# Kernel optimization log

Measured on AMD Instinct MI355X. Metric: run time of the kernel, lower is better.

## Reference

```python
import jax, jax.numpy as jnp
import numpy as np
import math

INPUT_DIM = 1024
OUTPUT_DIM = 8192
M_BLOCKS = 8  # ceil(OUTPUT_DIM / INPUT_DIM)
SCALE = 1.0


def fwht(x):
    """Unnormalized fast Walsh-Hadamard transform over the last axis.
    Matches the torch recursive-cat implementation (Sylvester/natural order).
    """
    n = x.shape[-1]
    lead = x.shape[:-1]
    h = 1
    while h < n:
        y = x.reshape(lead + (n // (2 * h), 2, h))
        a = y[..., 0, :]
        b = y[..., 1, :]
        x = jnp.stack([a + b, a - b], axis=-2).reshape(lead + (n,))
        h *= 2
    return x


def setup_inputs() -> dict:
    key = jax.random.key(0)
    kx, kb, kg, ks, kp, ku = jax.random.split(key, 6)
    x = jax.random.normal(kx, (8, 1024, INPUT_DIM), dtype=jnp.float32)
    B = jax.random.normal(kb, (M_BLOCKS, INPUT_DIM), dtype=jnp.float32)
    G = jax.random.normal(kg, (M_BLOCKS, INPUT_DIM), dtype=jnp.float32)
    S = jax.random.uniform(ks, (M_BLOCKS, INPUT_DIM), dtype=jnp.float32)
    P = jax.random.randint(kp, (M_BLOCKS, INPUT_DIM), 0, INPUT_DIM, dtype=jnp.int64)
    u_rand = jax.random.uniform(ku, (OUTPUT_DIM,), dtype=jnp.float32)
    return {"x": x, "B": B, "G": G, "S": S, "P": P, "u_rand": u_rand}


def reference(x, B, G, S, P, u_rand):
    d = INPUT_DIM
    # flatten all leading dims into rows: (R, 1, d)
    xr = x.reshape(-1, 1, d)
    Bx = xr * B                                   # (R, m, d)
    HBx = fwht(Bx)                                # (R, m, d)
    idx = jnp.broadcast_to(P[None], HBx.shape)    # per-block permutation gather
    PHBx = jnp.take_along_axis(HBx, idx, axis=-1)
    GPHBx = PHBx * G
    HGPHBx = fwht(GPHBx)
    SHGPHBx = HGPHBx * S
    norm_factor = 1.0 / (SCALE * math.sqrt(d))
    Vx = norm_factor * SHGPHBx.reshape(SHGPHBx.shape[0], -1)  # (R, m*d)
    result = Vx[:, :OUTPUT_DIM]
    # phi nonlinearity: cos(x + 2*pi*U) * sqrt(2/output_dim)
    phase = (2.0 * jnp.pi) * u_rand
    result = jnp.cos(result + phase) * math.sqrt(2.0 / OUTPUT_DIM)
    return result
```

## Files before the change

kernel.cpp:

```cpp
#include <hip/hip_runtime.h>
#include <math.h>


typedef unsigned uint2_ev __attribute__((ext_vector_type(2)));
typedef float    f32x4    __attribute__((ext_vector_type(4)));

template <int CTRL>
__device__ __forceinline__ float dpp_f(float x) {
    return __int_as_float(
        __builtin_amdgcn_mov_dpp(__float_as_int(x), CTRL, 0xF, 0xF, true));
}

#define DPP_XOR1 0xB1
#define DPP_XOR2 0x4E
#define DPP_XOR3 0x1B
#define DPP_HMIR 0x141
#define DPP_ROR8 0x128

__device__ __forceinline__ void fwht_full(float v[16], float sg0, float sg1,
                                          float sg2, float sg3, float sg4,
                                          float sg5) {
    (void)sg4; (void)sg5;
#pragma unroll
    for (int h = 1; h < 16; h <<= 1) {
#pragma unroll
        for (int k = 0; k < 16; ++k) {
            if (!(k & h)) {
                float a = v[k], b = v[k ^ h];
                v[k] = a + b;
                v[k ^ h] = a - b;
            }
        }
    }
#pragma unroll
    for (int k = 0; k < 16; ++k) v[k] = fmaf(v[k], sg0, dpp_f<DPP_XOR1>(v[k]));
#pragma unroll
    for (int k = 0; k < 16; ++k) v[k] = fmaf(v[k], sg1, dpp_f<DPP_XOR2>(v[k]));
#pragma unroll
    for (int k = 0; k < 16; ++k)
        v[k] = fmaf(v[k], sg2, dpp_f<DPP_XOR3>(dpp_f<DPP_HMIR>(v[k])));
#pragma unroll
    for (int k = 0; k < 16; ++k) v[k] = fmaf(v[k], sg3, dpp_f<DPP_ROR8>(v[k]));

#if __has_builtin(__builtin_amdgcn_permlane16_swap)
#pragma unroll
    for (int p = 0; p < 8; ++p) {
        uint2_ev r = __builtin_amdgcn_permlane16_swap(
            __float_as_uint(v[2 * p]), __float_as_uint(v[2 * p + 1]), false,
            false);
        float s = __uint_as_float(r.x) + __uint_as_float(r.y);
        float d = __uint_as_float(r.x) - __uint_as_float(r.y);
        uint2_ev q = __builtin_amdgcn_permlane16_swap(
            __float_as_uint(s), __float_as_uint(d), false, false);
        v[2 * p]     = __uint_as_float(q.x);
        v[2 * p + 1] = __uint_as_float(q.y);
    }
#else
#pragma unroll
    for (int k = 0; k < 16; ++k) {
        float t = __int_as_float(
            __builtin_amdgcn_ds_swizzle(__float_as_int(v[k]), 0x401F));
        v[k] = fmaf(v[k], sg4, t);
    }
#endif

#if __has_builtin(__builtin_amdgcn_permlane32_swap)
#pragma unroll
    for (int p = 0; p < 8; ++p) {
        uint2_ev r = __builtin_amdgcn_permlane32_swap(
            __float_as_uint(v[2 * p]), __float_as_uint(v[2 * p + 1]), false,
            false);
        float s = __uint_as_float(r.x) + __uint_as_float(r.y);
        float d = __uint_as_float(r.x) - __uint_as_float(r.y);
        uint2_ev q = __builtin_amdgcn_permlane32_swap(
            __float_as_uint(s), __float_as_uint(d), false, false);
        v[2 * p]     = __uint_as_float(q.x);
        v[2 * p + 1] = __uint_as_float(q.y);
    }
#else
#pragma unroll
    for (int k = 0; k < 16; ++k) {
        float t = __shfl_xor(v[k], 32, 64);
        v[k] = fmaf(v[k], sg5, t);
    }
#endif
}

__global__ __launch_bounds__(256) void fastfood_kernel(
    const float* __restrict__ x, const float* __restrict__ B,
    const float* __restrict__ G, const float* __restrict__ S,
    const int* __restrict__ P, const float* __restrict__ u_rand,
    float* __restrict__ out)
{
    __shared__ float lds[4 * 1088];
    const int lane = threadIdx.x & 63;
    const int wv   = threadIdx.x >> 6;
    const int row  = blockIdx.x * 4 + wv;

    const float sg0 = (lane & 1)  ? -1.f : 1.f;
    const float sg1 = (lane & 2)  ? -1.f : 1.f;
    const float sg2 = (lane & 4)  ? -1.f : 1.f;
    const float sg3 = (lane & 8)  ? -1.f : 1.f;
    const float sg4 = (lane & 16) ? -1.f : 1.f;
    const float sg5 = (lane & 32) ? -1.f : 1.f;

    float* wlds = lds + wv * 1088;
    float4* w4L1 = (float4*)(wlds + 16 * lane + 4 * (lane >> 2));

    const float c_arg = 0.03125f * 0.15915494309189535f;
    const float c_amp = 0.015625f;

    float xv[16];
    {
        const f32x4* x4 =
            (const f32x4*)(x + (size_t)row * 1024 + 16 * lane);
#pragma unroll
        for (int j = 0; j < 4; ++j) {
            f32x4 t = __builtin_nontemporal_load(&x4[j]);
            xv[4 * j + 0] = t.x; xv[4 * j + 1] = t.y;
            xv[4 * j + 2] = t.z; xv[4 * j + 3] = t.w;
        }
    }

#pragma unroll 1
    for (int m = 0; m < 8; ++m) {
        const int mo = m * 1024;
        float v[16];

        {
            const float4* B4 = (const float4*)(B + mo + 16 * lane);
#pragma unroll
            for (int j = 0; j < 4; ++j) {
                float4 b = B4[j];
                v[4 * j + 0] = xv[4 * j + 0] * b.x;
                v[4 * j + 1] = xv[4 * j + 1] * b.y;
                v[4 * j + 2] = xv[4 * j + 2] * b.z;
                v[4 * j + 3] = xv[4 * j + 3] * b.w;
            }
        }

        fwht_full(v, sg0, sg1, sg2, sg3, sg4, sg5);

        const int4*   P4 = (const int4*)(P + mo);
        const float4* G4 = (const float4*)(G + mo);
        int4   pj[4];
        float4 gj[4];
#pragma unroll
        for (int j = 0; j < 4; ++j) {
            pj[j] = P4[64 * j + lane];
            gj[j] = G4[64 * j + lane];
        }

#pragma unroll
        for (int j = 0; j < 4; ++j)
            w4L1[j] = make_float4(v[4 * j + 0], v[4 * j + 1],
                                  v[4 * j + 2], v[4 * j + 3]);

#pragma unroll
        for (int j = 0; j < 4; ++j) {
            int4 p = pj[j];
            float4 g = gj[j];
            v[4 * j + 0] = wlds[p.x + ((p.x >> 6) << 2)] * g.x;
            v[4 * j + 1] = wlds[p.y + ((p.y >> 6) << 2)] * g.y;
            v[4 * j + 2] = wlds[p.z + ((p.z >> 6) << 2)] * g.z;
            v[4 * j + 3] = wlds[p.w + ((p.w >> 6) << 2)] * g.w;
        }

        fwht_full(v, sg0, sg1, sg2, sg3, sg4, sg5);

        {
            const float4* S4 = (const float4*)(S + mo);
            const float4* U4 = (const float4*)(u_rand + mo);
            f32x4* o4 = (f32x4*)(out + (size_t)row * 8192 + mo);
#pragma unroll
            for (int b = 0; b < 4; ++b) {
                int idx = b * 64 + lane;
                float4 sv = S4[idx], uv = U4[idx];
                f32x4 rr;
                rr.x = __builtin_amdgcn_cosf(__builtin_amdgcn_fractf(
                           fmaf(v[4 * b + 0] * sv.x, c_arg, uv.x))) * c_amp;
                rr.y = __builtin_amdgcn_cosf(__builtin_amdgcn_fractf(
                           fmaf(v[4 * b + 1] * sv.y, c_arg, uv.y))) * c_amp;
                rr.z = __builtin_amdgcn_cosf(__builtin_amdgcn_fractf(
                           fmaf(v[4 * b + 2] * sv.z, c_arg, uv.z))) * c_amp;
                rr.w = __builtin_amdgcn_cosf(__builtin_amdgcn_fractf(
                           fmaf(v[4 * b + 3] * sv.w, c_arg, uv.w))) * c_amp;
                __builtin_nontemporal_store(rr, &o4[idx]);
            }
        }
    }
}

extern "C" void kernel_launch(void* const* d_in, const int* in_sizes, int n_in,
                              void* d_out, int out_size, void* d_ws, size_t ws_size,
                              hipStream_t stream) {
    const float* x = (const float*)d_in[0];
    const float* B = (const float*)d_in[1];
    const float* G = (const float*)d_in[2];
    const float* S = (const float*)d_in[3];
    const int*   P = (const int*)d_in[4];
    const float* u = (const float*)d_in[5];
    float* out = (float*)d_out;

    dim3 grid(2048), block(256);
    hipLaunchKernelGGL(fastfood_kernel, grid, block, 0, stream,
                       x, B, G, S, P, u, out);
}
```

Baseline: 345.3 us.

## Process two rows per wavefront to share B/P/G/S/U loads and add ILP

Each wavefront now handles two rows at once, interleaving their Walsh-Hadamard transforms so the per-block B, P, G, S and u_rand loads are shared and the DPP/permlane chains of the two rows can overlap. The grid is halved, LDS per block doubles, and launch bounds now request 3 blocks per CU. The aim is fewer redundant parameter loads and more instruction-level parallelism to hide shuffle latency. In exchange, register pressure rises and occupancy may drop. The non-permlane fallback paths are also removed.

```diff
diff --git a/kernel.cpp b/kernel.cpp
--- a/kernel.cpp
+++ b/kernel.cpp
@@ -17,129 +17,138 @@
 #define DPP_HMIR 0x141
 #define DPP_ROR8 0x128
 
-__device__ __forceinline__ void fwht_full(float v[16], float sg0, float sg1,
-                                          float sg2, float sg3, float sg4,
-                                          float sg5) {
-    (void)sg4; (void)sg5;
+__device__ __forceinline__ void pl16_pair(float& e0, float& e1) {
+    uint2_ev r = __builtin_amdgcn_permlane16_swap(
+        __float_as_uint(e0), __float_as_uint(e1), false, false);
+    float s = __uint_as_float(r.x) + __uint_as_float(r.y);
+    float d = __uint_as_float(r.x) - __uint_as_float(r.y);
+    uint2_ev q = __builtin_amdgcn_permlane16_swap(
+        __float_as_uint(s), __float_as_uint(d), false, false);
+    e0 = __uint_as_float(q.x);
+    e1 = __uint_as_float(q.y);
+}
+
+__device__ __forceinline__ void pl32_pair(float& e0, float& e1) {
+    uint2_ev r = __builtin_amdgcn_permlane32_swap(
+        __float_as_uint(e0), __float_as_uint(e1), false, false);
+    float s = __uint_as_float(r.x) + __uint_as_float(r.y);
+    float d = __uint_as_float(r.x) - __uint_as_float(r.y);
+    uint2_ev q = __builtin_amdgcn_permlane32_swap(
+        __float_as_uint(s), __float_as_uint(d), false, false);
+    e0 = __uint_as_float(q.x);
+    e1 = __uint_as_float(q.y);
+}
+
+__device__ __forceinline__ void fwht2(float a[16], float b[16], float sg0,
+                                      float sg1, float sg2, float sg3) {
 #pragma unroll
     for (int h = 1; h < 16; h <<= 1) {
 #pragma unroll
         for (int k = 0; k < 16; ++k) {
             if (!(k & h)) {
-                float a = v[k], b = v[k ^ h];
-                v[k] = a + b;
-                v[k ^ h] = a - b;
+                float t0 = a[k], t1 = a[k ^ h];
+                a[k] = t0 + t1;
+                a[k ^ h] = t0 - t1;
+                float u0 = b[k], u1 = b[k ^ h];
+                b[k] = u0 + u1;
+                b[k ^ h] = u0 - u1;
             }
         }
     }
 #pragma unroll
-    for (int k = 0; k < 16; ++k) v[k] = fmaf(v[k], sg0, dpp_f<DPP_XOR1>(v[k]));
-#pragma unroll
-    for (int k = 0; k < 16; ++k) v[k] = fmaf(v[k], sg1, dpp_f<DPP_XOR2>(v[k]));
-#pragma unroll
-    for (int k = 0; k < 16; ++k)
-        v[k] = fmaf(v[k], sg2, dpp_f<DPP_XOR3>(dpp_f<DPP_HMIR>(v[k])));
-#pragma unroll
-    for (int k = 0; k < 16; ++k) v[k] = fmaf(v[k], sg3, dpp_f<DPP_ROR8>(v[k]));
-
-#if __has_builtin(__builtin_amdgcn_permlane16_swap)
+    for (int k = 0; k < 16; ++k) {
+        a[k] = fmaf(a[k], sg0, dpp_f<DPP_XOR1>(a[k]));
+        b[k] = fmaf(b[k], sg0, dpp_f<DPP_XOR1>(b[k]));
+    }
+#pragma unroll
+    for (int k = 0; k < 16; ++k) {
+        a[k] = fmaf(a[k], sg1, dpp_f<DPP_XOR2>(a[k]));
+        b[k] = fmaf(b[k], sg1, dpp_f<DPP_XOR2>(b[k]));
+    }
+#pragma unroll
+    for (int k = 0; k < 16; ++k) {
+        a[k] = fmaf(a[k], sg2, dpp_f<DPP_XOR3>(dpp_f<DPP_HMIR>(a[k])));
+        b[k] = fmaf(b[k], sg2, dpp_f<DPP_XOR3>(dpp_f<DPP_HMIR>(b[k])));
+    }
+#pragma unroll
+    for (int k = 0; k < 16; ++k) {
+        a[k] = fmaf(a[k], sg3, dpp_f<DPP_ROR8>(a[k]));
+        b[k] = fmaf(b[k], sg3, dpp_f<DPP_ROR8>(b[k]));
+    }
 #pragma unroll
     for (int p = 0; p < 8; ++p) {
-        uint2_ev r = __builtin_amdgcn_permlane16_swap(
-            __float_as_uint(v[2 * p]), __float_as_uint(v[2 * p + 1]), false,
-            false);
-        float s = __uint_as_float(r.x) + __uint_as_float(r.y);
-        float d = __uint_as_float(r.x) - __uint_as_float(r.y);
-        uint2_ev q = __builtin_amdgcn_permlane16_swap(
-            __float_as_uint(s), __float_as_uint(d), false, false);
-        v[2 * p]     = __uint_as_float(q.x);
-        v[2 * p + 1] = __uint_as_float(q.y);
-    }
-#else
-#pragma unroll
-    for (int k = 0; k < 16; ++k) {
-        float t = __int_as_float(
-            __builtin_amdgcn_ds_swizzle(__float_as_int(v[k]), 0x401F));
-        v[k] = fmaf(v[k], sg4, t);
-    }
-#endif
-
-#if __has_builtin(__builtin_amdgcn_permlane32_swap)
+        pl16_pair(a[2 * p], a[2 * p + 1]);
+        pl16_pair(b[2 * p], b[2 * p + 1]);
+    }
 #pragma unroll
     for (int p = 0; p < 8; ++p) {
-        uint2_ev r = __builtin_amdgcn_permlane32_swap(
-            __float_as_uint(v[2 * p]), __float_as_uint(v[2 * p + 1]), false,
-            false);
-        float s = __uint_as_float(r.x) + __uint_as_float(r.y);
-        float d = __uint_as_float(r.x) - __uint_as_float(r.y);
-        uint2_ev q = __builtin_amdgcn_permlane32_swap(
-            __float_as_uint(s), __float_as_uint(d), false, false);
-        v[2 * p]     = __uint_as_float(q.x);
-        v[2 * p + 1] = __uint_as_float(q.y);
-    }
-#else
-#pragma unroll
-    for (int k = 0; k < 16; ++k) {
-        float t = __shfl_xor(v[k], 32, 64);
-        v[k] = fmaf(v[k], sg5, t);
-    }
-#endif
-}
-
-__global__ __launch_bounds__(256) void fastfood_kernel(
+        pl32_pair(a[2 * p], a[2 * p + 1]);
+        pl32_pair(b[2 * p], b[2 * p + 1]);
+    }
+}
+
+__global__ __launch_bounds__(256, 3) void fastfood_kernel(
     const float* __restrict__ x, const float* __restrict__ B,
     const float* __restrict__ G, const float* __restrict__ S,
     const int* __restrict__ P, const float* __restrict__ u_rand,
     float* __restrict__ out)
 {
-    __shared__ float lds[4 * 1088];
+    __shared__ float lds[4 * 2176];
     const int lane = threadIdx.x & 63;
     const int wv   = threadIdx.x >> 6;
-    const int row  = blockIdx.x * 4 + wv;
-
-    const float sg0 = (lane & 1)  ? -1.f : 1.f;
-    const float sg1 = (lane & 2)  ? -1.f : 1.f;
-    const float sg2 = (lane & 4)  ? -1.f : 1.f;
-    const float sg3 = (lane & 8)  ? -1.f : 1.f;
-    const float sg4 = (lane & 16) ? -1.f : 1.f;
-    const float sg5 = (lane & 32) ? -1.f : 1.f;
-
-    float* wlds = lds + wv * 1088;
-    float4* w4L1 = (float4*)(wlds + 16 * lane + 4 * (lane >> 2));
+    const int row  = blockIdx.x * 8 + wv * 2;
+
+    const float sg0 = (lane & 1) ? -1.f : 1.f;
+    const float sg1 = (lane & 2) ? -1.f : 1.f;
+    const float sg2 = (lane & 4) ? -1.f : 1.f;
+    const float sg3 = (lane & 8) ? -1.f : 1.f;
+
+    float* ldsA = lds + wv * 2176;
+    float* ldsB = ldsA + 1088;
+    const int woff = 16 * lane + 4 * (lane >> 2);
+    float4* wA = (float4*)(ldsA + woff);
+    float4* wB = (float4*)(ldsB + woff);
 
     const float c_arg = 0.03125f * 0.15915494309189535f;
     const float c_amp = 0.015625f;
 
-    float xv[16];
+    float xvA[16], xvB[16];
     {
-        const f32x4* x4 =
-            (const f32x4*)(x + (size_t)row * 1024 + 16 * lane);
-#pragma unroll
-        for (int j = 0; j < 4; ++j) {
-            f32x4 t = __builtin_nontemporal_load(&x4[j]);
-            xv[4 * j + 0] = t.x; xv[4 * j + 1] = t.y;
-            xv[4 * j + 2] = t.z; xv[4 * j + 3] = t.w;
+        const f32x4* xa = (const f32x4*)(x + (size_t)row * 1024 + 16 * lane);
+        const f32x4* xb = (const f32x4*)(x + (size_t)(row + 1) * 1024 + 16 * lane);
+#pragma unroll
+        for (int j = 0; j < 4; ++j) {
+            f32x4 t = __builtin_nontemporal_load(&xa[j]);
+            xvA[4 * j + 0] = t.x; xvA[4 * j + 1] = t.y;
+            xvA[4 * j + 2] = t.z; xvA[4 * j + 3] = t.w;
+            f32x4 u = __builtin_nontemporal_load(&xb[j]);
+            xvB[4 * j + 0] = u.x; xvB[4 * j + 1] = u.y;
+            xvB[4 * j + 2] = u.z; xvB[4 * j + 3] = u.w;
         }
     }
 
 #pragma unroll 1
     for (int m = 0; m < 8; ++m) {
         const int mo = m * 1024;
-        float v[16];
+        float vA[16], vB[16];
 
         {
             const float4* B4 = (const float4*)(B + mo + 16 * lane);
 #pragma unroll
             for (int j = 0; j < 4; ++j) {
-                float4 b = B4[j];
-                v[4 * j + 0] = xv[4 * j + 0] * b.x;
-                v[4 * j + 1] = xv[4 * j + 1] * b.y;
-                v[4 * j + 2] = xv[4 * j + 2] * b.z;
-                v[4 * j + 3] = xv[4 * j + 3] * b.w;
+                float4 bb = B4[j];
+                vA[4 * j + 0] = xvA[4 * j + 0] * bb.x;
+                vA[4 * j + 1] = xvA[4 * j + 1] * bb.y;
+                vA[4 * j + 2] = xvA[4 * j + 2] * bb.z;
+                vA[4 * j + 3] = xvA[4 * j + 3] * bb.w;
+                vB[4 * j + 0] = xvB[4 * j + 0] * bb.x;
+                vB[4 * j + 1] = xvB[4 * j + 1] * bb.y;
+                vB[4 * j + 2] = xvB[4 * j + 2] * bb.z;
+                vB[4 * j + 3] = xvB[4 * j + 3] * bb.w;
             }
         }
 
-        fwht_full(v, sg0, sg1, sg2, sg3, sg4, sg5);
+        fwht2(vA, vB, sg0, sg1, sg2, sg3);
 
         const int4*   P4 = (const int4*)(P + mo);
         const float4* G4 = (const float4*)(G + mo);
@@ -152,40 +161,61 @@
         }
 
 #pragma unroll
-        for (int j = 0; j < 4; ++j)
-            w4L1[j] = make_float4(v[4 * j + 0], v[4 * j + 1],
-                                  v[4 * j + 2], v[4 * j + 3]);
+        for (int j = 0; j < 4; ++j) {
+            wA[j] = make_float4(vA[4 * j + 0], vA[4 * j + 1],
+                                vA[4 * j + 2], vA[4 * j + 3]);
+            wB[j] = make_float4(vB[4 * j + 0], vB[4 * j + 1],
+                                vB[4 * j + 2], vB[4 * j + 3]);
+        }
 
 #pragma unroll
         for (int j = 0; j < 4; ++j) {
             int4 p = pj[j];
             float4 g = gj[j];
-            v[4 * j + 0] = wlds[p.x + ((p.x >> 6) << 2)] * g.x;
-            v[4 * j + 1] = wlds[p.y + ((p.y >> 6) << 2)] * g.y;
-            v[4 * j + 2] = wlds[p.z + ((p.z >> 6) << 2)] * g.z;
-            v[4 * j + 3] = wlds[p.w + ((p.w >> 6) << 2)] * g.w;
-        }
-
-        fwht_full(v, sg0, sg1, sg2, sg3, sg4, sg5);
+            int o0 = p.x + ((p.x >> 6) << 2);
+            int o1 = p.y + ((p.y >> 6) << 2);
+            int o2 = p.z + ((p.z >> 6) << 2);
+            int o3 = p.w + ((p.w >> 6) << 2);
+            vA[4 * j + 0] = ldsA[o0] * g.x;
+            vA[4 * j + 1] = ldsA[o1] * g.y;
+            vA[4 * j + 2] = ldsA[o2] * g.z;
+            vA[4 * j + 3] = ldsA[o3] * g.w;
+            vB[4 * j + 0] = ldsB[o0] * g.x;
+            vB[4 * j + 1] = ldsB[o1] * g.y;
+            vB[4 * j + 2] = ldsB[o2] * g.z;
+            vB[4 * j + 3] = ldsB[o3] * g.w;
+        }
+
+        fwht2(vA, vB, sg0, sg1, sg2, sg3);
 
         {
             const float4* S4 = (const float4*)(S + mo);
             const float4* U4 = (const float4*)(u_rand + mo);
-            f32x4* o4 = (f32x4*)(out + (size_t)row * 8192 + mo);
+            f32x4* oA = (f32x4*)(out + (size_t)row * 8192 + mo);
+            f32x4* oB = (f32x4*)(out + (size_t)(row + 1) * 8192 + mo);
 #pragma unroll
             for (int b = 0; b < 4; ++b) {
                 int idx = b * 64 + lane;
                 float4 sv = S4[idx], uv = U4[idx];
-                f32x4 rr;
-                rr.x = __builtin_amdgcn_cosf(__builtin_amdgcn_fractf(
-                           fmaf(v[4 * b + 0] * sv.x, c_arg, uv.x))) * c_amp;
-                rr.y = __builtin_amdgcn_cosf(__builtin_amdgcn_fractf(
-                           fmaf(v[4 * b + 1] * sv.y, c_arg, uv.y))) * c_amp;
-                rr.z = __builtin_amdgcn_cosf(__builtin_amdgcn_fractf(
-                           fmaf(v[4 * b + 2] * sv.z, c_arg, uv.z))) * c_amp;
-                rr.w = __builtin_amdgcn_cosf(__builtin_amdgcn_fractf(
-                           fmaf(v[4 * b + 3] * sv.w, c_arg, uv.w))) * c_amp;
-                __builtin_nontemporal_store(rr, &o4[idx]);
+                f32x4 ra, rb;
+                ra.x = __builtin_amdgcn_cosf(__builtin_amdgcn_fractf(
+                           fmaf(vA[4 * b + 0] * sv.x, c_arg, uv.x))) * c_amp;
+                ra.y = __builtin_amdgcn_cosf(__builtin_amdgcn_fractf(
+                           fmaf(vA[4 * b + 1] * sv.y, c_arg, uv.y))) * c_amp;
+                ra.z = __builtin_amdgcn_cosf(__builtin_amdgcn_fractf(
+                           fmaf(vA[4 * b + 2] * sv.z, c_arg, uv.z))) * c_amp;
+                ra.w = __builtin_amdgcn_cosf(__builtin_amdgcn_fractf(
+                           fmaf(vA[4 * b + 3] * sv.w, c_arg, uv.w))) * c_amp;
+                rb.x = __builtin_amdgcn_cosf(__builtin_amdgcn_fractf(
+                           fmaf(vB[4 * b + 0] * sv.x, c_arg, uv.x))) * c_amp;
+                rb.y = __builtin_amdgcn_cosf(__builtin_amdgcn_fractf(
+                           fmaf(vB[4 * b + 1] * sv.y, c_arg, uv.y))) * c_amp;
+                rb.z = __builtin_amdgcn_cosf(__builtin_amdgcn_fractf(
+                           fmaf(vB[4 * b + 2] * sv.z, c_arg, uv.z))) * c_amp;
+                rb.w = __builtin_amdgcn_cosf(__builtin_amdgcn_fractf(
+                           fmaf(vB[4 * b + 3] * sv.w, c_arg, uv.w))) * c_amp;
+                __builtin_nontemporal_store(ra, &oA[idx]);
+                __builtin_nontemporal_store(rb, &oB[idx]);
             }
         }
     }
@@ -202,7 +232,7 @@
     const float* u = (const float*)d_in[5];
     float* out = (float*)d_out;
 
-    dim3 grid(2048), block(256);
+    dim3 grid(1024), block(256);
     hipLaunchKernelGGL(fastfood_kernel, grid, block, 0, stream,
                        x, B, G, S, P, u, out);
 }
```

Measured after the change: 335.7 us (median of 2 runs). -2.8%, faster.

## Assign one wave per (row, block) pair and prefetch S/U before second FWHT

Applied to the files above, without the earlier changes.

Each wave now handles a single row and a single one of the 8 Hadamard blocks, replacing the serial 8-iteration loop, and the grid grows from 2048 to 16384 workgroups. This exposes more parallelism and shortens each wave's dependency chain. The cost is that each x row is reloaded eight times, now with plain rather than nontemporal loads, and more workgroup launches are needed. S and u_rand are loaded before the second transform to hide their latency, and the fallback paths for the permlane swap builtins are removed.

```diff
diff --git a/kernel.cpp b/kernel.cpp
--- a/kernel.cpp
+++ b/kernel.cpp
@@ -17,10 +17,30 @@
 #define DPP_HMIR 0x141
 #define DPP_ROR8 0x128
 
+__device__ __forceinline__ void pl16_pair(float& e0, float& e1) {
+    uint2_ev r = __builtin_amdgcn_permlane16_swap(
+        __float_as_uint(e0), __float_as_uint(e1), false, false);
+    float s = __uint_as_float(r.x) + __uint_as_float(r.y);
+    float d = __uint_as_float(r.x) - __uint_as_float(r.y);
+    uint2_ev q = __builtin_amdgcn_permlane16_swap(
+        __float_as_uint(s), __float_as_uint(d), false, false);
+    e0 = __uint_as_float(q.x);
+    e1 = __uint_as_float(q.y);
+}
+
+__device__ __forceinline__ void pl32_pair(float& e0, float& e1) {
+    uint2_ev r = __builtin_amdgcn_permlane32_swap(
+        __float_as_uint(e0), __float_as_uint(e1), false, false);
+    float s = __uint_as_float(r.x) + __uint_as_float(r.y);
+    float d = __uint_as_float(r.x) - __uint_as_float(r.y);
+    uint2_ev q = __builtin_amdgcn_permlane32_swap(
+        __float_as_uint(s), __float_as_uint(d), false, false);
+    e0 = __uint_as_float(q.x);
+    e1 = __uint_as_float(q.y);
+}
+
 __device__ __forceinline__ void fwht_full(float v[16], float sg0, float sg1,
-                                          float sg2, float sg3, float sg4,
-                                          float sg5) {
-    (void)sg4; (void)sg5;
+                                          float sg2, float sg3) {
 #pragma unroll
     for (int h = 1; h < 16; h <<= 1) {
 #pragma unroll
@@ -41,49 +61,10 @@
         v[k] = fmaf(v[k], sg2, dpp_f<DPP_XOR3>(dpp_f<DPP_HMIR>(v[k])));
 #pragma unroll
     for (int k = 0; k < 16; ++k) v[k] = fmaf(v[k], sg3, dpp_f<DPP_ROR8>(v[k]));
-
-#if __has_builtin(__builtin_amdgcn_permlane16_swap)
 #pragma unroll
-    for (int p = 0; p < 8; ++p) {
-        uint2_ev r = __builtin_amdgcn_permlane16_swap(
-            __float_as_uint(v[2 * p]), __float_as_uint(v[2 * p + 1]), false,
-            false);
-        float s = __uint_as_float(r.x) + __uint_as_float(r.y);
-        float d = __uint_as_float(r.x) - __uint_as_float(r.y);
-        uint2_ev q = __builtin_amdgcn_permlane16_swap(
-            __float_as_uint(s), __float_as_uint(d), false, false);
-        v[2 * p]     = __uint_as_float(q.x);
-        v[2 * p + 1] = __uint_as_float(q.y);
-    }
-#else
+    for (int p = 0; p < 8; ++p) pl16_pair(v[2 * p], v[2 * p + 1]);
 #pragma unroll
-    for (int k = 0; k < 16; ++k) {
-        float t = __int_as_float(
-            __builtin_amdgcn_ds_swizzle(__float_as_int(v[k]), 0x401F));
-        v[k] = fmaf(v[k], sg4, t);
-    }
-#endif
-
-#if __has_builtin(__builtin_amdgcn_permlane32_swap)
-#pragma unroll
-    for (int p = 0; p < 8; ++p) {
-        uint2_ev r = __builtin_amdgcn_permlane32_swap(
-            __float_as_uint(v[2 * p]), __float_as_uint(v[2 * p + 1]), false,
-            false);
-        float s = __uint_as_float(r.x) + __uint_as_float(r.y);
-        float d = __uint_as_float(r.x) - __uint_as_float(r.y);
-        uint2_ev q = __builtin_amdgcn_permlane32_swap(
-            __float_as_uint(s), __float_as_uint(d), false, false);
-        v[2 * p]     = __uint_as_float(q.x);
-        v[2 * p + 1] = __uint_as_float(q.y);
-    }
-#else
-#pragma unroll
-    for (int k = 0; k < 16; ++k) {
-        float t = __shfl_xor(v[k], 32, 64);
-        v[k] = fmaf(v[k], sg5, t);
-    }
-#endif
+    for (int p = 0; p < 8; ++p) pl32_pair(v[2 * p], v[2 * p + 1]);
 }
 
 __global__ __launch_bounds__(256) void fastfood_kernel(
@@ -95,98 +76,93 @@
     __shared__ float lds[4 * 1088];
     const int lane = threadIdx.x & 63;
     const int wv   = threadIdx.x >> 6;
-    const int row  = blockIdx.x * 4 + wv;
+    const int gw   = blockIdx.x * 4 + wv;
+    const int row  = gw >> 3;
+    const int mo   = (gw & 7) << 10;
 
-    const float sg0 = (lane & 1)  ? -1.f : 1.f;
-    const float sg1 = (lane & 2)  ? -1.f : 1.f;
-    const float sg2 = (lane & 4)  ? -1.f : 1.f;
-    const float sg3 = (lane & 8)  ? -1.f : 1.f;
-    const float sg4 = (lane & 16) ? -1.f : 1.f;
-    const float sg5 = (lane & 32) ? -1.f : 1.f;
+    const float sg0 = (lane & 1) ? -1.f : 1.f;
+    const float sg1 = (lane & 2) ? -1.f : 1.f;
+    const float sg2 = (lane & 4) ? -1.f : 1.f;
+    const float sg3 = (lane & 8) ? -1.f : 1.f;
 
     float* wlds = lds + wv * 1088;
-    float4* w4L1 = (float4*)(wlds + 16 * lane + 4 * (lane >> 2));
+    float4* w4 = (float4*)(wlds + 16 * lane + 4 * (lane >> 2));
 
     const float c_arg = 0.03125f * 0.15915494309189535f;
     const float c_amp = 0.015625f;
 
-    float xv[16];
+    float v[16];
+
     {
-        const f32x4* x4 =
-            (const f32x4*)(x + (size_t)row * 1024 + 16 * lane);
+        const float4* x4 = (const float4*)(x + (size_t)row * 1024 + 16 * lane);
+        const float4* B4 = (const float4*)(B + mo + 16 * lane);
 #pragma unroll
         for (int j = 0; j < 4; ++j) {
-            f32x4 t = __builtin_nontemporal_load(&x4[j]);
-            xv[4 * j + 0] = t.x; xv[4 * j + 1] = t.y;
-            xv[4 * j + 2] = t.z; xv[4 * j + 3] = t.w;
+            float4 xt = x4[j];
+            float4 bt = B4[j];
+            v[4 * j + 0] = xt.x * bt.x;
+            v[4 * j + 1] = xt.y * bt.y;
+            v[4 * j + 2] = xt.z * bt.z;
+            v[4 * j + 3] = xt.w * bt.w;
         }
     }
 
-#pragma unroll 1
-    for (int m = 0; m < 8; ++m) {
-        const int mo = m * 1024;
-        float v[16];
+    fwht_full(v, sg0, sg1, sg2, sg3);
 
-        {
-            const float4* B4 = (const float4*)(B + mo + 16 * lane);
+    const int4*   P4 = (const int4*)(P + mo);
+    const float4* G4 = (const float4*)(G + mo);
+    int4   pj[4];
+    float4 gj[4];
 #pragma unroll
-            for (int j = 0; j < 4; ++j) {
-                float4 b = B4[j];
-                v[4 * j + 0] = xv[4 * j + 0] * b.x;
-                v[4 * j + 1] = xv[4 * j + 1] * b.y;
-                v[4 * j + 2] = xv[4 * j + 2] * b.z;
-                v[4 * j + 3] = xv[4 * j + 3] * b.w;
-            }
-        }
-
-        fwht_full(v, sg0, sg1, sg2, sg3, sg4, sg5);
-
-        const int4*   P4 = (const int4*)(P + mo);
-        const float4* G4 = (const float4*)(G + mo);
-        int4   pj[4];
-        float4 gj[4];
-#pragma unroll
-        for (int j = 0; j < 4; ++j) {
-            pj[j] = P4[64 * j + lane];
-            gj[j] = G4[64 * j + lane];
-        }
+    for (int j = 0; j < 4; ++j) {
+        pj[j] = P4[64 * j + lane];
+        gj[j] = G4[64 * j + lane];
+    }
 
 #pragma unroll
-        for (int j = 0; j < 4; ++j)
-            w4L1[j] = make_float4(v[4 * j + 0], v[4 * j + 1],
-                                  v[4 * j + 2], v[4 * j + 3]);
+    for (int j = 0; j < 4; ++j)
+        w4[j] = make_float4(v[4 * j + 0], v[4 * j + 1],
+                            v[4 * j + 2], v[4 * j + 3]);
 
 #pragma unroll
-        for (int j = 0; j < 4; ++j) {
-            int4 p = pj[j];
-            float4 g = gj[j];
-            v[4 * j + 0] = wlds[p.x + ((p.x >> 6) << 2)] * g.x;
-            v[4 * j + 1] = wlds[p.y + ((p.y >> 6) << 2)] * g.y;
-            v[4 * j + 2] = wlds[p.z + ((p.z >> 6) << 2)] * g.z;
-            v[4 * j + 3] = wlds[p.w + ((p.w >> 6) << 2)] * g.w;
+    for (int j = 0; j < 4; ++j) {
+        int4 p = pj[j];
+        float4 g = gj[j];
+        v[4 * j + 0] = wlds[p.x + ((p.x >> 6) << 2)] * g.x;
+        v[4 * j + 1] = wlds[p.y + ((p.y >> 6) << 2)] * g.y;
+        v[4 * j + 2] = wlds[p.z + ((p.z >> 6) << 2)] * g.z;
+        v[4 * j + 3] = wlds[p.w + ((p.w >> 6) << 2)] * g.w;
+    }
+
+    float4 sv[4], uv[4];
+    {
+        const float4* S4 = (const float4*)(S + mo);
+        const float4* U4 = (const float4*)(u_rand + mo);
+#pragma unroll
+        for (int b = 0; b < 4; ++b) {
+            int idx = b * 64 + lane;
+            sv[b] = S4[idx];
+            uv[b] = U4[idx];
         }
+    }
 
-        fwht_full(v, sg0, sg1, sg2, sg3, sg4, sg5);
+    fwht_full(v, sg0, sg1, sg2, sg3);
 
-        {
-            const float4* S4 = (const float4*)(S + mo);
-            const float4* U4 = (const float4*)(u_rand + mo);
-            f32x4* o4 = (f32x4*)(out + (size_t)row * 8192 + mo);
+    {
+        f32x4* o4 = (f32x4*)(out + (size_t)row * 8192 + mo);
 #pragma unroll
-            for (int b = 0; b < 4; ++b) {
-                int idx = b * 64 + lane;
-                float4 sv = S4[idx], uv = U4[idx];
-                f32x4 rr;
-                rr.x = __builtin_amdgcn_cosf(__builtin_amdgcn_fractf(
-                           fmaf(v[4 * b + 0] * sv.x, c_arg, uv.x))) * c_amp;
-                rr.y = __builtin_amdgcn_cosf(__builtin_amdgcn_fractf(
-                           fmaf(v[4 * b + 1] * sv.y, c_arg, uv.y))) * c_amp;
-                rr.z = __builtin_amdgcn_cosf(__builtin_amdgcn_fractf(
-                           fmaf(v[4 * b + 2] * sv.z, c_arg, uv.z))) * c_amp;
-                rr.w = __builtin_amdgcn_cosf(__builtin_amdgcn_fractf(
-                           fmaf(v[4 * b + 3] * sv.w, c_arg, uv.w))) * c_amp;
-                __builtin_nontemporal_store(rr, &o4[idx]);
-            }
+        for (int b = 0; b < 4; ++b) {
+            int idx = b * 64 + lane;
+            f32x4 rr;
+            rr.x = __builtin_amdgcn_cosf(__builtin_amdgcn_fractf(
+                       fmaf(v[4 * b + 0] * sv[b].x, c_arg, uv[b].x))) * c_amp;
+            rr.y = __builtin_amdgcn_cosf(__builtin_amdgcn_fractf(
+                       fmaf(v[4 * b + 1] * sv[b].y, c_arg, uv[b].y))) * c_amp;
+            rr.z = __builtin_amdgcn_cosf(__builtin_amdgcn_fractf(
+                       fmaf(v[4 * b + 2] * sv[b].z, c_arg, uv[b].z))) * c_amp;
+            rr.w = __builtin_amdgcn_cosf(__builtin_amdgcn_fractf(
+                       fmaf(v[4 * b + 3] * sv[b].w, c_arg, uv[b].w))) * c_amp;
+            __builtin_nontemporal_store(rr, &o4[idx]);
         }
     }
 }
@@ -202,7 +178,7 @@
     const float* u = (const float*)d_in[5];
     float* out = (float*)d_out;
 
-    dim3 grid(2048), block(256);
+    dim3 grid(16384), block(256);
     hipLaunchKernelGGL(fastfood_kernel, grid, block, 0, stream,
                        x, B, G, S, P, u, out);
 }
```

New measurement: 342.1 us. Within noise of the previous version (-0.9%).
